# Performance work log

Hardware: AMD Instinct MI355X
Metric: run time of the kernel (lower is better)

Reference implementation:

```python
import jax, jax.numpy as jnp
import numpy as np

H = 2048      # hidden_size
NH = 16       # num heads
HD = H // NH  # head_dim = 128


def setup_inputs() -> dict:
    key = jax.random.key(0)
    ks = jax.random.split(key, 5)
    x = jax.random.normal(ks[0], (2, 2048, H), dtype=jnp.float32)
    # qkv_proj: Linear(H, 3H) with bias; out_proj: Linear(H, H) with bias
    s = 1.0 / np.sqrt(H)
    w_qkv = jax.random.uniform(ks[1], (3 * H, H), jnp.float32, -s, s)
    b_qkv = jax.random.uniform(ks[2], (3 * H,), jnp.float32, -s, s)
    w_out = jax.random.uniform(ks[3], (H, H), jnp.float32, -s, s)
    b_out = jax.random.uniform(ks[4], (H,), jnp.float32, -s, s)
    return {"x": x, "w_qkv": w_qkv, "b_qkv": b_qkv, "w_out": w_out, "b_out": b_out}


def reference(x, w_qkv, b_qkv, w_out, b_out):
    b, s, _ = x.shape
    # fused QKV projection: [b, s, 3H]
    xqkv = jnp.einsum('bsh,oh->bso', x, w_qkv) + b_qkv
    xqkv = xqkv.reshape(b, s, 3, NH, HD)
    q = xqkv[:, :, 0].transpose(0, 2, 1, 3)  # [b, nh, s, hd]
    k = xqkv[:, :, 1].transpose(0, 2, 1, 3)
    v = xqkv[:, :, 2].transpose(0, 2, 1, 3)
    # non-causal SDPA (attn_mask=None, is_causal=False)
    scores = jnp.einsum('bhqd,bhkd->bhqk', q, k) / np.sqrt(HD).astype(np.float32)
    attn = jax.nn.softmax(scores, axis=-1)
    out = jnp.einsum('bhqk,bhkd->bhqd', attn, v)
    out = out.transpose(0, 2, 1, 3).reshape(b, s, NH * HD)
    return jnp.einsum('bsh,oh->bso', out, w_out) + b_out
```

## Files before the change

### kernel.cpp

```cpp
#include <hip/hip_runtime.h>
#include <hip/hip_bf16.h>


typedef __bf16 bf16x8 __attribute__((ext_vector_type(8)));
typedef float f32x4 __attribute__((ext_vector_type(4)));
typedef unsigned short ushort8_t __attribute__((ext_vector_type(8)));
typedef unsigned short ushort4_t __attribute__((ext_vector_type(4)));

__device__ __forceinline__ unsigned short f2bf(float f) {
  unsigned int u = __float_as_uint(f);
  u += 0x7fffu + ((u >> 16) & 1u);
  return (unsigned short)(u >> 16);
}

__device__ __forceinline__ unsigned int pk2bf(float lo, float hi) {
  unsigned int a = (__float_as_uint(lo) + 0x8000u) >> 16;
  unsigned int b = (__float_as_uint(hi) + 0x8000u) & 0xffff0000u;
  return a | b;
}

__device__ __forceinline__ float fexp2(float x) {
#if __has_builtin(__builtin_amdgcn_exp2f)
  return __builtin_amdgcn_exp2f(x);
#else
  return exp2f(x);
#endif
}

__device__ __forceinline__ f32x4 mfma16(bf16x8 a, bf16x8 b, f32x4 c) {
  return __builtin_amdgcn_mfma_f32_16x16x32_bf16(a, b, c, 0, 0, 0);
}

__device__ __forceinline__ void gload_lds16(const void* g, void* lds) {
  __builtin_amdgcn_global_load_lds(
      (const __attribute__((address_space(1))) unsigned int*)g,
      (__attribute__((address_space(3))) unsigned int*)lds, 16, 0, 0);
}

__global__ __launch_bounds__(256) void f32_to_bf16_k(const float* __restrict__ in,
                                                     unsigned short* __restrict__ out,
                                                     int n) {
  int i = (blockIdx.x * 256 + threadIdx.x) * 8;
  if (i >= n) return;
  float4 a = *(const float4*)(in + i);
  float4 b = *(const float4*)(in + i + 4);
  ushort8_t o;
  o[0] = f2bf(a.x); o[1] = f2bf(a.y); o[2] = f2bf(a.z); o[3] = f2bf(a.w);
  o[4] = f2bf(b.x); o[5] = f2bf(b.y); o[6] = f2bf(b.z); o[7] = f2bf(b.w);
  *(ushort8_t*)(out + i) = o;
}

template <int OUT_MODE>
__global__ __launch_bounds__(256) void gemm_nt(const unsigned short* __restrict__ A,
                                               const unsigned short* __restrict__ B,
                                               const float* __restrict__ bias,
                                               void* __restrict__ Cout,
                                               int Ns, int K) {
  __shared__ __attribute__((aligned(16))) unsigned short As[128 * 64];
  __shared__ __attribute__((aligned(16))) unsigned short Bs[128 * 64];
  const int tid = threadIdx.x;
  const int lane = tid & 63;
  const int wv = tid >> 6;
  const int wm = wv >> 1, wn = wv & 1;
  const int lr = lane & 15, lg = lane >> 4;
  const int m0 = blockIdx.y * 128, n0 = blockIdx.x * 128;

  f32x4 acc[4][4];
#pragma unroll
  for (int i = 0; i < 4; ++i)
#pragma unroll
    for (int j = 0; j < 4; ++j) acc[i][j] = (f32x4){0.f, 0.f, 0.f, 0.f};

  for (int kt = 0; kt < K; kt += 64) {
    __syncthreads();
#pragma unroll
    for (int i = 0; i < 4; ++i) {
      int c = i * 256 + tid;
      int r = c >> 3;
      int lc = (c & 7) ^ (r & 7);
      gload_lds16(A + (size_t)(m0 + r) * K + kt + lc * 8, &As[c * 8]);
      gload_lds16(B + (size_t)(n0 + r) * K + kt + lc * 8, &Bs[c * 8]);
    }
    __syncthreads();
#pragma unroll
    for (int kk = 0; kk < 64; kk += 32) {
      bf16x8 af[4], bf[4];
#pragma unroll
      for (int i = 0; i < 4; ++i) {
        int pcA = ((kk >> 3) + lg) ^ (lr & 7);
        af[i] = *(const bf16x8*)&As[(wm * 64 + i * 16 + lr) * 64 + pcA * 8];
        bf[i] = *(const bf16x8*)&Bs[(wn * 64 + i * 16 + lr) * 64 + pcA * 8];
      }
#pragma unroll
      for (int i = 0; i < 4; ++i)
#pragma unroll
        for (int j = 0; j < 4; ++j) acc[i][j] = mfma16(af[i], bf[j], acc[i][j]);
    }
  }

#pragma unroll
  for (int j = 0; j < 4; ++j) {
    int n = n0 + wn * 64 + j * 16 + lr;
    float bv = bias[n];
#pragma unroll
    for (int i = 0; i < 4; ++i) {
      int mbase = m0 + wm * 64 + i * 16 + lg * 4;
      if (OUT_MODE == 2) {
        int hh = n >> 7, dd = n & 127;
        int b = mbase >> 11, s = mbase & 2047;
        ushort4_t o4;
#pragma unroll
        for (int r = 0; r < 4; ++r) o4[r] = f2bf(acc[i][j][r] + bv);
        *(ushort4_t*)&((unsigned short*)Cout)[((size_t)((b * 16 + hh) * 128 + dd)) * 2048 + s] = o4;
      } else {
#pragma unroll
        for (int r = 0; r < 4; ++r) {
          float v = acc[i][j][r] + bv;
          if (OUT_MODE == 1)
            ((unsigned short*)Cout)[(size_t)(mbase + r) * Ns + n] = f2bf(v);
          else
            ((float*)Cout)[(size_t)(mbase + r) * Ns + n] = v;
        }
      }
    }
  }
}

__device__ __forceinline__ void stage_tiles(const unsigned short* __restrict__ qkv,
                                            const unsigned short* __restrict__ vbase,
                                            int b, int h, int t, int tid,
                                            unsigned short* KsB, unsigned short* VtB) {
  const int s0k = t * 64;
  const int krow = b * 2048 + s0k;
#pragma unroll
  for (int i = 0; i < 4; ++i) {
    int c = i * 256 + tid;
    int r = c >> 4;
    int lc = (c & 15) ^ (r & 15);
    gload_lds16(qkv + (size_t)(krow + r) * 6144 + 2048 + h * 128 + lc * 8, &KsB[c * 8]);
  }
#pragma unroll
  for (int i = 0; i < 4; ++i) {
    int c = i * 256 + tid;
    int r = c >> 3;
    int lc = (c & 7) ^ (r & 7);
    gload_lds16(vbase + (size_t)r * 2048 + s0k + lc * 8, &VtB[c * 8]);
  }
}

__global__ __launch_bounds__(256, 2) void flash_attn(const unsigned short* __restrict__ qkv,
                                                     const unsigned short* __restrict__ vT,
                                                     unsigned short* __restrict__ attnb) {
  __shared__ __attribute__((aligned(16))) unsigned short Ks0[64 * 128];
  __shared__ __attribute__((aligned(16))) unsigned short Ks1[64 * 128];
  __shared__ __attribute__((aligned(16))) unsigned short Vt0[128 * 64];
  __shared__ __attribute__((aligned(16))) unsigned short Vt1[128 * 64];

  const int tid = threadIdx.x;
  const int lane = tid & 63;
  const int w = tid >> 6;
  const int bh = blockIdx.y;
  const int b = bh >> 4, h = bh & 15;
  const int q0 = blockIdx.x * 128;
  const int lr = lane & 15, lg = lane >> 4;
  const float cs = 0.08838834764831845f * 1.44269504088896340f;

  const unsigned short* vbase = vT + (size_t)bh * 128 * 2048;

  bf16x8 qf[2][4];
#pragma unroll
  for (int g = 0; g < 2; ++g) {
    int m = b * 2048 + q0 + w * 32 + g * 16 + lr;
    const unsigned short* qrow = qkv + (size_t)m * 6144 + h * 128;
#pragma unroll
    for (int kb = 0; kb < 4; ++kb) qf[g][kb] = *(const bf16x8*)(qrow + kb * 32 + lg * 8);
  }

  float l_i[2] = {0.f, 0.f};
  f32x4 O[2][8];
#pragma unroll
  for (int g = 0; g < 2; ++g)
#pragma unroll
    for (int nb = 0; nb < 8; ++nb) O[g][nb] = (f32x4){0.f, 0.f, 0.f, 0.f};

  unsigned short* Kc = Ks0;  unsigned short* Kn = Ks1;
  unsigned short* Vc = Vt0;  unsigned short* Vn = Vt1;

  stage_tiles(qkv, vbase, b, h, 0, tid, Kc, Vc);

  for (int t = 0; t < 32; ++t) {
    __syncthreads();
    if (t + 1 < 32) stage_tiles(qkv, vbase, b, h, t + 1, tid, Kn, Vn);

    f32x4 sc[2][4];
#pragma unroll
    for (int g = 0; g < 2; ++g)
#pragma unroll
      for (int cb = 0; cb < 4; ++cb) sc[g][cb] = (f32x4){0.f, 0.f, 0.f, 0.f};
    __builtin_amdgcn_s_setprio(1);
#pragma unroll
    for (int cb = 0; cb < 4; ++cb) {
#pragma unroll
      for (int kb = 0; kb < 4; ++kb) {
        int pc = (kb * 4 + lg) ^ lr;
        bf16x8 kf = *(const bf16x8*)&Kc[(cb * 16 + lr) * 128 + pc * 8];
        sc[0][cb] = mfma16(kf, qf[0][kb], sc[0][cb]);
        sc[1][cb] = mfma16(kf, qf[1][kb], sc[1][cb]);
      }
    }
    __builtin_amdgcn_s_setprio(0);

    unsigned int pk[2][4][2];
#pragma unroll
    for (int g = 0; g < 2; ++g) {
      float rs = 0.f;
#pragma unroll
      for (int cb = 0; cb < 4; ++cb) {
        float p0 = fexp2(sc[g][cb][0] * cs);
        float p1 = fexp2(sc[g][cb][1] * cs);
        float p2 = fexp2(sc[g][cb][2] * cs);
        float p3 = fexp2(sc[g][cb][3] * cs);
        rs += (p0 + p1) + (p2 + p3);
        pk[g][cb][0] = pk2bf(p0, p1);
        pk[g][cb][1] = pk2bf(p2, p3);
      }
      rs += __shfl_xor(rs, 16, 64);
      rs += __shfl_xor(rs, 32, 64);
      l_i[g] += rs;
    }

#pragma unroll
    for (int kb2 = 0; kb2 < 2; ++kb2) {
      bf16x8 pf[2];
#pragma unroll
      for (int g = 0; g < 2; ++g) {
        unsigned int a0 = pk[g][2 * kb2 + 0][0];
        unsigned int b0 = pk[g][2 * kb2 + 1][0];
        unsigned int a1 = pk[g][2 * kb2 + 0][1];
        unsigned int b1 = pk[g][2 * kb2 + 1][1];
        asm("v_permlane32_swap_b32 %0, %1" : "+v"(a0), "+v"(b0));
        asm("v_permlane16_swap_b32 %0, %1" : "+v"(a0), "+v"(b0));
        asm("v_permlane32_swap_b32 %0, %1" : "+v"(a1), "+v"(b1));
        asm("v_permlane16_swap_b32 %0, %1" : "+v"(a1), "+v"(b1));
        uint4 u;
        u.x = a0;
        u.y = a1;
        u.z = b0;
        u.w = b1;
        pf[g] = *(bf16x8*)&u;
      }
      __builtin_amdgcn_s_setprio(1);
#pragma unroll
      for (int nb = 0; nb < 8; ++nb) {
        int pc = (kb2 * 4 + lg) ^ (lr & 7);
        bf16x8 vtf = *(const bf16x8*)&Vc[(nb * 16 + lr) * 64 + pc * 8];
        O[0][nb] = mfma16(vtf, pf[0], O[0][nb]);
        O[1][nb] = mfma16(vtf, pf[1], O[1][nb]);
      }
      __builtin_amdgcn_s_setprio(0);
    }

    unsigned short* tk = Kc; Kc = Kn; Kn = tk;
    unsigned short* tv = Vc; Vc = Vn; Vn = tv;
  }

#pragma unroll
  for (int g = 0; g < 2; ++g) {
    int m = b * 2048 + q0 + w * 32 + g * 16 + lr;
    float inv = 1.0f / l_i[g];
    unsigned short* orow = attnb + (size_t)m * 2048 + h * 128;
#pragma unroll
    for (int nb = 0; nb < 8; ++nb) {
      ushort4_t o4;
#pragma unroll
      for (int r = 0; r < 4; ++r) o4[r] = f2bf(O[g][nb][r] * inv);
      *(ushort4_t*)&orow[nb * 16 + lg * 4] = o4;
    }
  }
}

extern "C" void kernel_launch(void* const* d_in, const int* in_sizes, int n_in,
                              void* d_out, int out_size, void* d_ws, size_t ws_size,
                              hipStream_t stream) {
  const float* x = (const float*)d_in[0];
  const float* w_qkv = (const float*)d_in[1];
  const float* b_qkv = (const float*)d_in[2];
  const float* w_out = (const float*)d_in[3];
  const float* b_out = (const float*)d_in[4];
  float* out = (float*)d_out;

  char* ws = (char*)d_ws;
  unsigned short* xb = (unsigned short*)ws;
  unsigned short* attnb = xb;
  unsigned short* wqkvb = (unsigned short*)(ws + (16u << 20));
  unsigned short* woutb = wqkvb;
  unsigned short* qkvb = (unsigned short*)(ws + (40u << 20));
  unsigned short* vT = (unsigned short*)(ws + (88u << 20));

  f32_to_bf16_k<<<8388608 / 2048, 256, 0, stream>>>(x, xb, 8388608);
  f32_to_bf16_k<<<12582912 / 2048, 256, 0, stream>>>(w_qkv, wqkvb, 12582912);

  gemm_nt<1><<<dim3(32, 32), 256, 0, stream>>>(xb, wqkvb, b_qkv, qkvb, 6144, 2048);
  gemm_nt<2><<<dim3(16, 32), 256, 0, stream>>>(xb, wqkvb + (size_t)4096 * 2048,
                                               b_qkv + 4096, vT, 2048, 2048);

  f32_to_bf16_k<<<4194304 / 2048, 256, 0, stream>>>(w_out, woutb, 4194304);

  flash_attn<<<dim3(16, 32), 256, 0, stream>>>(qkvb, vT, attnb);

  gemm_nt<0><<<dim3(16, 32), 256, 0, stream>>>(attnb, woutb, b_out, out, 2048, 2048);
}
```

Before: 393.5 us.

## Split attention over two KV halves with partial-sum reduction kernel

Adds a split-KV flash attention kernel launched with a z dimension of 2. Each block processes half of the key/value tiles and writes unnormalized fp32 partial outputs and row sums to workspace, and a separate reduction kernel combines them, normalizes, and writes bf16. This doubles the grid from 512 blocks to get better CU occupancy, and uses single-buffered LDS with launch bounds of 4 blocks per SM. In exchange it adds extra fp32 traffic for the partials, a second kernel launch, and loses the double-buffered load overlap; the old kernel is kept as a fallback when the workspace is too small.

```diff
diff --git a/kernel.cpp b/kernel.cpp
--- a/kernel.cpp
+++ b/kernel.cpp
@@ -148,18 +148,18 @@
   }
 }
 
-__global__ __launch_bounds__(256, 2) void flash_attn(const unsigned short* __restrict__ qkv,
-                                                     const unsigned short* __restrict__ vT,
-                                                     unsigned short* __restrict__ attnb) {
-  __shared__ __attribute__((aligned(16))) unsigned short Ks0[64 * 128];
-  __shared__ __attribute__((aligned(16))) unsigned short Ks1[64 * 128];
-  __shared__ __attribute__((aligned(16))) unsigned short Vt0[128 * 64];
-  __shared__ __attribute__((aligned(16))) unsigned short Vt1[128 * 64];
+__global__ __launch_bounds__(256, 4) void flash_split(const unsigned short* __restrict__ qkv,
+                                                      const unsigned short* __restrict__ vT,
+                                                      float* __restrict__ PO,
+                                                      float* __restrict__ PL) {
+  __shared__ __attribute__((aligned(16))) unsigned short Ks[64 * 128];
+  __shared__ __attribute__((aligned(16))) unsigned short Vt[128 * 64];
 
   const int tid = threadIdx.x;
   const int lane = tid & 63;
   const int w = tid >> 6;
   const int bh = blockIdx.y;
+  const int z = blockIdx.z;
   const int b = bh >> 4, h = bh & 15;
   const int q0 = blockIdx.x * 128;
   const int lr = lane & 15, lg = lane >> 4;
@@ -183,14 +183,10 @@
 #pragma unroll
     for (int nb = 0; nb < 8; ++nb) O[g][nb] = (f32x4){0.f, 0.f, 0.f, 0.f};
 
-  unsigned short* Kc = Ks0;  unsigned short* Kn = Ks1;
-  unsigned short* Vc = Vt0;  unsigned short* Vn = Vt1;
-
-  stage_tiles(qkv, vbase, b, h, 0, tid, Kc, Vc);
-
-  for (int t = 0; t < 32; ++t) {
+  for (int t = z * 16; t < z * 16 + 16; ++t) {
     __syncthreads();
-    if (t + 1 < 32) stage_tiles(qkv, vbase, b, h, t + 1, tid, Kn, Vn);
+    stage_tiles(qkv, vbase, b, h, t, tid, Ks, Vt);
+    __syncthreads();
 
     f32x4 sc[2][4];
 #pragma unroll
@@ -203,7 +199,7 @@
 #pragma unroll
       for (int kb = 0; kb < 4; ++kb) {
         int pc = (kb * 4 + lg) ^ lr;
-        bf16x8 kf = *(const bf16x8*)&Kc[(cb * 16 + lr) * 128 + pc * 8];
+        bf16x8 kf = *(const bf16x8*)&Ks[(cb * 16 + lr) * 128 + pc * 8];
         sc[0][cb] = mfma16(kf, qf[0][kb], sc[0][cb]);
         sc[1][cb] = mfma16(kf, qf[1][kb], sc[1][cb]);
       }
@@ -243,10 +239,147 @@
         asm("v_permlane32_swap_b32 %0, %1" : "+v"(a1), "+v"(b1));
         asm("v_permlane16_swap_b32 %0, %1" : "+v"(a1), "+v"(b1));
         uint4 u;
-        u.x = a0;
-        u.y = a1;
-        u.z = b0;
-        u.w = b1;
+        u.x = a0; u.y = a1; u.z = b0; u.w = b1;
+        pf[g] = *(bf16x8*)&u;
+      }
+      __builtin_amdgcn_s_setprio(1);
+#pragma unroll
+      for (int nb = 0; nb < 8; ++nb) {
+        int pc = (kb2 * 4 + lg) ^ (lr & 7);
+        bf16x8 vtf = *(const bf16x8*)&Vt[(nb * 16 + lr) * 64 + pc * 8];
+        O[0][nb] = mfma16(vtf, pf[0], O[0][nb]);
+        O[1][nb] = mfma16(vtf, pf[1], O[1][nb]);
+      }
+      __builtin_amdgcn_s_setprio(0);
+    }
+  }
+
+#pragma unroll
+  for (int g = 0; g < 2; ++g) {
+    int q = q0 + w * 32 + g * 16 + lr;
+    size_t prow = ((size_t)(z * 32 + bh) * 2048 + q) * 128;
+#pragma unroll
+    for (int nb = 0; nb < 8; ++nb)
+      *(f32x4*)&PO[prow + nb * 16 + lg * 4] = O[g][nb];
+    if (lg == 0) PL[(size_t)(z * 32 + bh) * 2048 + q] = l_i[g];
+  }
+}
+
+__global__ __launch_bounds__(256) void reduce_o_k(const float* __restrict__ PO,
+                                                  const float* __restrict__ PL,
+                                                  unsigned short* __restrict__ attnb) {
+  int idx = blockIdx.x * 256 + threadIdx.x;
+  int row = idx >> 5;
+  int d4 = (idx & 31) * 4;
+  float4 a = *(const float4*)&PO[((size_t)row << 7) + d4];
+  float4 c = *(const float4*)&PO[(((size_t)row + 65536) << 7) + d4];
+  float inv = 1.0f / (PL[row] + PL[row + 65536]);
+  ushort4_t o;
+  o[0] = f2bf((a.x + c.x) * inv);
+  o[1] = f2bf((a.y + c.y) * inv);
+  o[2] = f2bf((a.z + c.z) * inv);
+  o[3] = f2bf((a.w + c.w) * inv);
+  int bh = row >> 11, q = row & 2047;
+  int b = bh >> 4, h = bh & 15;
+  *(ushort4_t*)&attnb[((size_t)(b * 2048 + q)) * 2048 + h * 128 + d4] = o;
+}
+
+__global__ __launch_bounds__(256, 2) void flash_attn(const unsigned short* __restrict__ qkv,
+                                                     const unsigned short* __restrict__ vT,
+                                                     unsigned short* __restrict__ attnb) {
+  __shared__ __attribute__((aligned(16))) unsigned short Ks0[64 * 128];
+  __shared__ __attribute__((aligned(16))) unsigned short Ks1[64 * 128];
+  __shared__ __attribute__((aligned(16))) unsigned short Vt0[128 * 64];
+  __shared__ __attribute__((aligned(16))) unsigned short Vt1[128 * 64];
+
+  const int tid = threadIdx.x;
+  const int lane = tid & 63;
+  const int w = tid >> 6;
+  const int bh = blockIdx.y;
+  const int b = bh >> 4, h = bh & 15;
+  const int q0 = blockIdx.x * 128;
+  const int lr = lane & 15, lg = lane >> 4;
+  const float cs = 0.08838834764831845f * 1.44269504088896340f;
+
+  const unsigned short* vbase = vT + (size_t)bh * 128 * 2048;
+
+  bf16x8 qf[2][4];
+#pragma unroll
+  for (int g = 0; g < 2; ++g) {
+    int m = b * 2048 + q0 + w * 32 + g * 16 + lr;
+    const unsigned short* qrow = qkv + (size_t)m * 6144 + h * 128;
+#pragma unroll
+    for (int kb = 0; kb < 4; ++kb) qf[g][kb] = *(const bf16x8*)(qrow + kb * 32 + lg * 8);
+  }
+
+  float l_i[2] = {0.f, 0.f};
+  f32x4 O[2][8];
+#pragma unroll
+  for (int g = 0; g < 2; ++g)
+#pragma unroll
+    for (int nb = 0; nb < 8; ++nb) O[g][nb] = (f32x4){0.f, 0.f, 0.f, 0.f};
+
+  unsigned short* Kc = Ks0;  unsigned short* Kn = Ks1;
+  unsigned short* Vc = Vt0;  unsigned short* Vn = Vt1;
+
+  stage_tiles(qkv, vbase, b, h, 0, tid, Kc, Vc);
+
+  for (int t = 0; t < 32; ++t) {
+    __syncthreads();
+    if (t + 1 < 32) stage_tiles(qkv, vbase, b, h, t + 1, tid, Kn, Vn);
+
+    f32x4 sc[2][4];
+#pragma unroll
+    for (int g = 0; g < 2; ++g)
+#pragma unroll
+      for (int cb = 0; cb < 4; ++cb) sc[g][cb] = (f32x4){0.f, 0.f, 0.f, 0.f};
+    __builtin_amdgcn_s_setprio(1);
+#pragma unroll
+    for (int cb = 0; cb < 4; ++cb) {
+#pragma unroll
+      for (int kb = 0; kb < 4; ++kb) {
+        int pc = (kb * 4 + lg) ^ lr;
+        bf16x8 kf = *(const bf16x8*)&Kc[(cb * 16 + lr) * 128 + pc * 8];
+        sc[0][cb] = mfma16(kf, qf[0][kb], sc[0][cb]);
+        sc[1][cb] = mfma16(kf, qf[1][kb], sc[1][cb]);
+      }
+    }
+    __builtin_amdgcn_s_setprio(0);
+
+    unsigned int pk[2][4][2];
+#pragma unroll
+    for (int g = 0; g < 2; ++g) {
+      float rs = 0.f;
+#pragma unroll
+      for (int cb = 0; cb < 4; ++cb) {
+        float p0 = fexp2(sc[g][cb][0] * cs);
+        float p1 = fexp2(sc[g][cb][1] * cs);
+        float p2 = fexp2(sc[g][cb][2] * cs);
+        float p3 = fexp2(sc[g][cb][3] * cs);
+        rs += (p0 + p1) + (p2 + p3);
+        pk[g][cb][0] = pk2bf(p0, p1);
+        pk[g][cb][1] = pk2bf(p2, p3);
+      }
+      rs += __shfl_xor(rs, 16, 64);
+      rs += __shfl_xor(rs, 32, 64);
+      l_i[g] += rs;
+    }
+
+#pragma unroll
+    for (int kb2 = 0; kb2 < 2; ++kb2) {
+      bf16x8 pf[2];
+#pragma unroll
+      for (int g = 0; g < 2; ++g) {
+        unsigned int a0 = pk[g][2 * kb2 + 0][0];
+        unsigned int b0 = pk[g][2 * kb2 + 1][0];
+        unsigned int a1 = pk[g][2 * kb2 + 0][1];
+        unsigned int b1 = pk[g][2 * kb2 + 1][1];
+        asm("v_permlane32_swap_b32 %0, %1" : "+v"(a0), "+v"(b0));
+        asm("v_permlane16_swap_b32 %0, %1" : "+v"(a0), "+v"(b0));
+        asm("v_permlane32_swap_b32 %0, %1" : "+v"(a1), "+v"(b1));
+        asm("v_permlane16_swap_b32 %0, %1" : "+v"(a1), "+v"(b1));
+        uint4 u;
+        u.x = a0; u.y = a1; u.z = b0; u.w = b1;
         pf[g] = *(bf16x8*)&u;
       }
       __builtin_amdgcn_s_setprio(1);
@@ -306,7 +439,14 @@
 
   f32_to_bf16_k<<<4194304 / 2048, 256, 0, stream>>>(w_out, woutb, 4194304);
 
-  flash_attn<<<dim3(16, 32), 256, 0, stream>>>(qkvb, vT, attnb);
+  if (ws_size >= (169ull << 20)) {
+    float* PO = (float*)(ws + (104ull << 20));
+    float* PL = (float*)(ws + (168ull << 20));
+    flash_split<<<dim3(16, 32, 2), 256, 0, stream>>>(qkvb, vT, PO, PL);
+    reduce_o_k<<<8192, 256, 0, stream>>>(PO, PL, attnb);
+  } else {
+    flash_attn<<<dim3(16, 32), 256, 0, stream>>>(qkvb, vT, attnb);
+  }
 
   gemm_nt<0><<<dim3(16, 32), 256, 0, stream>>>(attnb, woutb, b_out, out, 2048, 2048);
 }
```

New measurement: 623.8 us. +58.5%, slower.

## Add 256x256-tile 512-thread GEMM for Q/K projection with split-phase staging

Applied to the files above, without the earlier changes.

Adds a new GEMM kernel using 256x256 output tiles, 8 waves and double-buffered LDS, where loads for the next A and B half-tiles are interleaved with the two k-phases of MFMA work. It replaces the previous QKV projection launch over the first 4096 columns (grid 16x16 covering N=4096 of Ns=6144). The aim is more operand reuse per LDS load and fewer blocks. The larger accumulator array (128 floats per thread) raises register pressure, and the 256-block grid may underfill the device.

```diff
diff --git a/kernel.cpp b/kernel.cpp
--- a/kernel.cpp
+++ b/kernel.cpp
@@ -126,6 +126,117 @@
   }
 }
 
+__device__ __forceinline__ void stage_half256(const unsigned short* __restrict__ src,
+                                              int K, unsigned short* lds, int half,
+                                              int tid) {
+#pragma unroll
+  for (int j = 0; j < 2; ++j) {
+    int c = half * 1024 + j * 512 + tid;
+    int r = c >> 3;
+    int lc = (c & 7) ^ (r & 7);
+    gload_lds16(src + (size_t)r * K + lc * 8, &lds[c * 8]);
+  }
+}
+
+__device__ __forceinline__ void phase256(const unsigned short* __restrict__ Ac,
+                                         const unsigned short* __restrict__ Bc,
+                                         int kk, int wm, int wn, int lr, int lg,
+                                         f32x4 acc[8][4]) {
+  bf16x8 a[8];
+  bf16x8 bb[4];
+  const int pc = ((kk >> 3) + lg) ^ (lr & 7);
+#pragma unroll
+  for (int i = 0; i < 8; ++i)
+    a[i] = *(const bf16x8*)&Ac[(wm * 128 + i * 16 + lr) * 64 + pc * 8];
+#pragma unroll
+  for (int j = 0; j < 4; ++j)
+    bb[j] = *(const bf16x8*)&Bc[(wn * 64 + j * 16 + lr) * 64 + pc * 8];
+  __builtin_amdgcn_s_setprio(1);
+#pragma unroll
+  for (int i = 0; i < 8; ++i)
+#pragma unroll
+    for (int j = 0; j < 4; ++j) acc[i][j] = mfma16(a[i], bb[j], acc[i][j]);
+  __builtin_amdgcn_s_setprio(0);
+}
+
+__global__ __launch_bounds__(512, 2) void gemm256_nt(const unsigned short* __restrict__ A,
+                                                     const unsigned short* __restrict__ B,
+                                                     const float* __restrict__ bias,
+                                                     unsigned short* __restrict__ C,
+                                                     int Ns, int K) {
+  __shared__ __attribute__((aligned(16))) unsigned short As0[256 * 64];
+  __shared__ __attribute__((aligned(16))) unsigned short As1[256 * 64];
+  __shared__ __attribute__((aligned(16))) unsigned short Bs0[256 * 64];
+  __shared__ __attribute__((aligned(16))) unsigned short Bs1[256 * 64];
+
+  const int tid = threadIdx.x;
+  const int lane = tid & 63;
+  const int w = tid >> 6;
+  const int wm = w >> 2, wn = w & 3;
+  const int lr = lane & 15, lg = lane >> 4;
+  const int m0 = blockIdx.y * 256, n0 = blockIdx.x * 256;
+
+  const unsigned short* Abase = A + (size_t)m0 * K;
+  const unsigned short* Bbase = B + (size_t)n0 * K;
+
+  f32x4 acc[8][4];
+#pragma unroll
+  for (int i = 0; i < 8; ++i)
+#pragma unroll
+    for (int j = 0; j < 4; ++j) acc[i][j] = (f32x4){0.f, 0.f, 0.f, 0.f};
+
+  unsigned short* Ac = As0;  unsigned short* An = As1;
+  unsigned short* Bc = Bs0;  unsigned short* Bn = Bs1;
+
+  stage_half256(Abase, K, Ac, 0, tid);
+  stage_half256(Abase, K, Ac, 1, tid);
+  stage_half256(Bbase, K, Bc, 0, tid);
+  stage_half256(Bbase, K, Bc, 1, tid);
+
+  const int nkt = K >> 6;
+  for (int t = 0; t < nkt; ++t) {
+    const int tn = (t + 1) & (nkt - 1);
+    const unsigned short* Asrc = Abase + tn * 64;
+    const unsigned short* Bsrc = Bbase + tn * 64;
+
+    stage_half256(Asrc, K, An, 0, tid);
+    stage_half256(Asrc, K, An, 1, tid);
+    asm volatile("s_waitcnt vmcnt(4)" ::: "memory");
+    __builtin_amdgcn_s_barrier();
+    __builtin_amdgcn_sched_barrier(0);
+
+    phase256(Ac, Bc, 0, wm, wn, lr, lg, acc);
+
+    stage_half256(Bsrc, K, Bn, 0, tid);
+    stage_half256(Bsrc, K, Bn, 1, tid);
+    asm volatile("" ::: "memory");
+    __builtin_amdgcn_s_barrier();
+    __builtin_amdgcn_sched_barrier(0);
+
+    phase256(Ac, Bc, 32, wm, wn, lr, lg, acc);
+
+    asm volatile("" ::: "memory");
+    __builtin_amdgcn_s_barrier();
+    __builtin_amdgcn_sched_barrier(0);
+
+    unsigned short* ta = Ac; Ac = An; An = ta;
+    unsigned short* tb = Bc; Bc = Bn; Bn = tb;
+  }
+
+#pragma unroll
+  for (int j = 0; j < 4; ++j) {
+    int n = n0 + wn * 64 + j * 16 + lr;
+    float bv = bias[n];
+#pragma unroll
+    for (int i = 0; i < 8; ++i) {
+      int mbase = m0 + wm * 128 + i * 16 + lg * 4;
+#pragma unroll
+      for (int r = 0; r < 4; ++r)
+        C[(size_t)(mbase + r) * Ns + n] = f2bf(acc[i][j][r] + bv);
+    }
+  }
+}
+
 __device__ __forceinline__ void stage_tiles(const unsigned short* __restrict__ qkv,
                                             const unsigned short* __restrict__ vbase,
                                             int b, int h, int t, int tid,
@@ -243,10 +354,7 @@
         asm("v_permlane32_swap_b32 %0, %1" : "+v"(a1), "+v"(b1));
         asm("v_permlane16_swap_b32 %0, %1" : "+v"(a1), "+v"(b1));
         uint4 u;
-        u.x = a0;
-        u.y = a1;
-        u.z = b0;
-        u.w = b1;
+        u.x = a0; u.y = a1; u.z = b0; u.w = b1;
         pf[g] = *(bf16x8*)&u;
       }
       __builtin_amdgcn_s_setprio(1);
@@ -300,7 +408,7 @@
   f32_to_bf16_k<<<8388608 / 2048, 256, 0, stream>>>(x, xb, 8388608);
   f32_to_bf16_k<<<12582912 / 2048, 256, 0, stream>>>(w_qkv, wqkvb, 12582912);
 
-  gemm_nt<1><<<dim3(32, 32), 256, 0, stream>>>(xb, wqkvb, b_qkv, qkvb, 6144, 2048);
+  gemm256_nt<<<dim3(16, 16), 512, 0, stream>>>(xb, wqkvb, b_qkv, qkvb, 6144, 2048);
   gemm_nt<2><<<dim3(16, 32), 256, 0, stream>>>(xb, wqkvb + (size_t)4096 * 2048,
                                                b_qkv + 4096, vT, 2048, 2048);
 
```

Result: no change. 397.1 us (+0.9%).

## Software-pipeline attention QK and PV across iterations and merge conversion kernels

Applied to the files above, without the earlier changes.

The flash attention loop is restructured so the QK^T scores for the next key tile are computed interleaved with the PV matmul of the current tile. K is prefetched two tiles ahead and V one tile ahead. The intent is to overlap the exp/softmax work with MFMA and hide latency. Separately, the three fp32-to-bf16 conversion launches are merged into one kernel, with w_out given its own workspace region, to cut launch overhead. The change adds register pressure (sc and pk are both live) and makes the loop more complex.

```diff
diff --git a/kernel.cpp b/kernel.cpp
--- a/kernel.cpp
+++ b/kernel.cpp
@@ -37,17 +37,28 @@
       (__attribute__((address_space(3))) unsigned int*)lds, 16, 0, 0);
 }
 
-__global__ __launch_bounds__(256) void f32_to_bf16_k(const float* __restrict__ in,
-                                                     unsigned short* __restrict__ out,
-                                                     int n) {
+__global__ __launch_bounds__(256) void cvt_all_k(const float* __restrict__ x,
+                                                 const float* __restrict__ wqkv,
+                                                 const float* __restrict__ wout,
+                                                 unsigned short* __restrict__ xb,
+                                                 unsigned short* __restrict__ wqkvb,
+                                                 unsigned short* __restrict__ woutb) {
   int i = (blockIdx.x * 256 + threadIdx.x) * 8;
-  if (i >= n) return;
-  float4 a = *(const float4*)(in + i);
-  float4 b = *(const float4*)(in + i + 4);
+  const float* in;
+  unsigned short* out;
+  if (i < 8388608) {
+    in = x + i; out = xb + i;
+  } else if (i < 20971520) {
+    in = wqkv + (i - 8388608); out = wqkvb + (i - 8388608);
+  } else {
+    in = wout + (i - 20971520); out = woutb + (i - 20971520);
+  }
+  float4 a = *(const float4*)(in);
+  float4 b = *(const float4*)(in + 4);
   ushort8_t o;
   o[0] = f2bf(a.x); o[1] = f2bf(a.y); o[2] = f2bf(a.z); o[3] = f2bf(a.w);
   o[4] = f2bf(b.x); o[5] = f2bf(b.y); o[6] = f2bf(b.z); o[7] = f2bf(b.w);
-  *(ushort8_t*)(out + i) = o;
+  *(ushort8_t*)(out) = o;
 }
 
 template <int OUT_MODE>
@@ -126,12 +137,10 @@
   }
 }
 
-__device__ __forceinline__ void stage_tiles(const unsigned short* __restrict__ qkv,
-                                            const unsigned short* __restrict__ vbase,
-                                            int b, int h, int t, int tid,
-                                            unsigned short* KsB, unsigned short* VtB) {
-  const int s0k = t * 64;
-  const int krow = b * 2048 + s0k;
+__device__ __forceinline__ void stage_K(const unsigned short* __restrict__ qkv,
+                                        int b, int h, int t, int tid,
+                                        unsigned short* KsB) {
+  const int krow = b * 2048 + t * 64;
 #pragma unroll
   for (int i = 0; i < 4; ++i) {
     int c = i * 256 + tid;
@@ -139,6 +148,11 @@
     int lc = (c & 15) ^ (r & 15);
     gload_lds16(qkv + (size_t)(krow + r) * 6144 + 2048 + h * 128 + lc * 8, &KsB[c * 8]);
   }
+}
+
+__device__ __forceinline__ void stage_V(const unsigned short* __restrict__ vbase,
+                                        int t, int tid, unsigned short* VtB) {
+  const int s0k = t * 64;
 #pragma unroll
   for (int i = 0; i < 4; ++i) {
     int c = i * 256 + tid;
@@ -183,15 +197,13 @@
 #pragma unroll
     for (int nb = 0; nb < 8; ++nb) O[g][nb] = (f32x4){0.f, 0.f, 0.f, 0.f};
 
-  unsigned short* Kc = Ks0;  unsigned short* Kn = Ks1;
-  unsigned short* Vc = Vt0;  unsigned short* Vn = Vt1;
-
-  stage_tiles(qkv, vbase, b, h, 0, tid, Kc, Vc);
-
-  for (int t = 0; t < 32; ++t) {
-    __syncthreads();
-    if (t + 1 < 32) stage_tiles(qkv, vbase, b, h, t + 1, tid, Kn, Vn);
-
+  stage_K(qkv, b, h, 0, tid, Ks0);
+  stage_V(vbase, 0, tid, Vt0);
+  stage_K(qkv, b, h, 1, tid, Ks1);
+  __syncthreads();
+
+  unsigned int pk[2][4][2];
+  {
     f32x4 sc[2][4];
 #pragma unroll
     for (int g = 0; g < 2; ++g)
@@ -203,14 +215,12 @@
 #pragma unroll
       for (int kb = 0; kb < 4; ++kb) {
         int pc = (kb * 4 + lg) ^ lr;
-        bf16x8 kf = *(const bf16x8*)&Kc[(cb * 16 + lr) * 128 + pc * 8];
+        bf16x8 kf = *(const bf16x8*)&Ks0[(cb * 16 + lr) * 128 + pc * 8];
         sc[0][cb] = mfma16(kf, qf[0][kb], sc[0][cb]);
         sc[1][cb] = mfma16(kf, qf[1][kb], sc[1][cb]);
       }
     }
     __builtin_amdgcn_s_setprio(0);
-
-    unsigned int pk[2][4][2];
 #pragma unroll
     for (int g = 0; g < 2; ++g) {
       float rs = 0.f;
@@ -228,40 +238,131 @@
       rs += __shfl_xor(rs, 32, 64);
       l_i[g] += rs;
     }
-
-#pragma unroll
-    for (int kb2 = 0; kb2 < 2; ++kb2) {
+  }
+
+  unsigned short* Kread = Ks1;  unsigned short* Kwrite = Ks0;
+  unsigned short* Vread = Vt0;  unsigned short* Vwrite = Vt1;
+
+  for (int i = 0; i < 32; ++i) {
+    __syncthreads();
+    if (i + 2 < 32) stage_K(qkv, b, h, i + 2, tid, Kwrite);
+    if (i + 1 < 32) stage_V(vbase, i + 1, tid, Vwrite);
+    const bool nx = (i + 1 < 32);
+
+    f32x4 sc[2][4];
+    if (nx) {
+#pragma unroll
+      for (int g = 0; g < 2; ++g)
+#pragma unroll
+        for (int cb = 0; cb < 4; ++cb) sc[g][cb] = (f32x4){0.f, 0.f, 0.f, 0.f};
+    }
+
+    if (nx) {
+      __builtin_amdgcn_s_setprio(1);
+#pragma unroll
+      for (int cb = 0; cb < 2; ++cb) {
+#pragma unroll
+        for (int kb = 0; kb < 4; ++kb) {
+          int pc = (kb * 4 + lg) ^ lr;
+          bf16x8 kf = *(const bf16x8*)&Kread[(cb * 16 + lr) * 128 + pc * 8];
+          sc[0][cb] = mfma16(kf, qf[0][kb], sc[0][cb]);
+          sc[1][cb] = mfma16(kf, qf[1][kb], sc[1][cb]);
+        }
+      }
+      __builtin_amdgcn_s_setprio(0);
+    }
+
+    {
       bf16x8 pf[2];
 #pragma unroll
       for (int g = 0; g < 2; ++g) {
-        unsigned int a0 = pk[g][2 * kb2 + 0][0];
-        unsigned int b0 = pk[g][2 * kb2 + 1][0];
-        unsigned int a1 = pk[g][2 * kb2 + 0][1];
-        unsigned int b1 = pk[g][2 * kb2 + 1][1];
+        unsigned int a0 = pk[g][0][0];
+        unsigned int b0 = pk[g][1][0];
+        unsigned int a1 = pk[g][0][1];
+        unsigned int b1 = pk[g][1][1];
         asm("v_permlane32_swap_b32 %0, %1" : "+v"(a0), "+v"(b0));
         asm("v_permlane16_swap_b32 %0, %1" : "+v"(a0), "+v"(b0));
         asm("v_permlane32_swap_b32 %0, %1" : "+v"(a1), "+v"(b1));
         asm("v_permlane16_swap_b32 %0, %1" : "+v"(a1), "+v"(b1));
         uint4 u;
-        u.x = a0;
-        u.y = a1;
-        u.z = b0;
-        u.w = b1;
+        u.x = a0; u.y = a1; u.z = b0; u.w = b1;
         pf[g] = *(bf16x8*)&u;
       }
       __builtin_amdgcn_s_setprio(1);
 #pragma unroll
       for (int nb = 0; nb < 8; ++nb) {
-        int pc = (kb2 * 4 + lg) ^ (lr & 7);
-        bf16x8 vtf = *(const bf16x8*)&Vc[(nb * 16 + lr) * 64 + pc * 8];
+        int pc = lg ^ (lr & 7);
+        bf16x8 vtf = *(const bf16x8*)&Vread[(nb * 16 + lr) * 64 + pc * 8];
         O[0][nb] = mfma16(vtf, pf[0], O[0][nb]);
         O[1][nb] = mfma16(vtf, pf[1], O[1][nb]);
       }
       __builtin_amdgcn_s_setprio(0);
     }
 
-    unsigned short* tk = Kc; Kc = Kn; Kn = tk;
-    unsigned short* tv = Vc; Vc = Vn; Vn = tv;
+    if (nx) {
+      __builtin_amdgcn_s_setprio(1);
+#pragma unroll
+      for (int cb = 2; cb < 4; ++cb) {
+#pragma unroll
+        for (int kb = 0; kb < 4; ++kb) {
+          int pc = (kb * 4 + lg) ^ lr;
+          bf16x8 kf = *(const bf16x8*)&Kread[(cb * 16 + lr) * 128 + pc * 8];
+          sc[0][cb] = mfma16(kf, qf[0][kb], sc[0][cb]);
+          sc[1][cb] = mfma16(kf, qf[1][kb], sc[1][cb]);
+        }
+      }
+      __builtin_amdgcn_s_setprio(0);
+    }
+
+    {
+      bf16x8 pf[2];
+#pragma unroll
+      for (int g = 0; g < 2; ++g) {
+        unsigned int a0 = pk[g][2][0];
+        unsigned int b0 = pk[g][3][0];
+        unsigned int a1 = pk[g][2][1];
+        unsigned int b1 = pk[g][3][1];
+        asm("v_permlane32_swap_b32 %0, %1" : "+v"(a0), "+v"(b0));
+        asm("v_permlane16_swap_b32 %0, %1" : "+v"(a0), "+v"(b0));
+        asm("v_permlane32_swap_b32 %0, %1" : "+v"(a1), "+v"(b1));
+        asm("v_permlane16_swap_b32 %0, %1" : "+v"(a1), "+v"(b1));
+        uint4 u;
+        u.x = a0; u.y = a1; u.z = b0; u.w = b1;
+        pf[g] = *(bf16x8*)&u;
+      }
+      __builtin_amdgcn_s_setprio(1);
+#pragma unroll
+      for (int nb = 0; nb < 8; ++nb) {
+        int pc = (4 + lg) ^ (lr & 7);
+        bf16x8 vtf = *(const bf16x8*)&Vread[(nb * 16 + lr) * 64 + pc * 8];
+        O[0][nb] = mfma16(vtf, pf[0], O[0][nb]);
+        O[1][nb] = mfma16(vtf, pf[1], O[1][nb]);
+      }
+      __builtin_amdgcn_s_setprio(0);
+    }
+
+    if (nx) {
+#pragma unroll
+      for (int g = 0; g < 2; ++g) {
+        float rs = 0.f;
+#pragma unroll
+        for (int cb = 0; cb < 4; ++cb) {
+          float p0 = fexp2(sc[g][cb][0] * cs);
+          float p1 = fexp2(sc[g][cb][1] * cs);
+          float p2 = fexp2(sc[g][cb][2] * cs);
+          float p3 = fexp2(sc[g][cb][3] * cs);
+          rs += (p0 + p1) + (p2 + p3);
+          pk[g][cb][0] = pk2bf(p0, p1);
+          pk[g][cb][1] = pk2bf(p2, p3);
+        }
+        rs += __shfl_xor(rs, 16, 64);
+        rs += __shfl_xor(rs, 32, 64);
+        l_i[g] += rs;
+      }
+    }
+
+    unsigned short* tk = Kread; Kread = Kwrite; Kwrite = tk;
+    unsigned short* tv = Vread; Vread = Vwrite; Vwrite = tv;
   }
 
 #pragma unroll
@@ -293,19 +394,16 @@
   unsigned short* xb = (unsigned short*)ws;
   unsigned short* attnb = xb;
   unsigned short* wqkvb = (unsigned short*)(ws + (16u << 20));
-  unsigned short* woutb = wqkvb;
   unsigned short* qkvb = (unsigned short*)(ws + (40u << 20));
   unsigned short* vT = (unsigned short*)(ws + (88u << 20));
-
-  f32_to_bf16_k<<<8388608 / 2048, 256, 0, stream>>>(x, xb, 8388608);
-  f32_to_bf16_k<<<12582912 / 2048, 256, 0, stream>>>(w_qkv, wqkvb, 12582912);
+  unsigned short* woutb = (unsigned short*)(ws + (104ull << 20));
+
+  cvt_all_k<<<25165824 / 2048, 256, 0, stream>>>(x, w_qkv, w_out, xb, wqkvb, woutb);
 
   gemm_nt<1><<<dim3(32, 32), 256, 0, stream>>>(xb, wqkvb, b_qkv, qkvb, 6144, 2048);
   gemm_nt<2><<<dim3(16, 32), 256, 0, stream>>>(xb, wqkvb + (size_t)4096 * 2048,
                                                b_qkv + 4096, vT, 2048, 2048);
 
-  f32_to_bf16_k<<<4194304 / 2048, 256, 0, stream>>>(w_out, woutb, 4194304);
-
   flash_attn<<<dim3(16, 32), 256, 0, stream>>>(qkvb, vT, attnb);
 
   gemm_nt<0><<<dim3(16, 32), 256, 0, stream>>>(attnb, woutb, b_out, out, 2048, 2048);
```

Result: faster. 385.4 us (-2.1%).
